# Kernel optimization log

Measured on AMD Instinct MI355X. Metric: run time of the kernel, lower is better.

## Reference

```python
import jax, jax.numpy as jnp
import numpy as np

L = 2048  # sequence length
V = 2048  # num_tokens == channel width (one-hot embedding)
B = 4     # batch


def _pos_bias(v_table):
    # pos[i,j] = max(i-j, 0); embed via [L,1] table -> [L,L]
    i = jnp.arange(L)
    pos = jnp.maximum(i[:, None] - i[None, :], 0)
    return v_table[pos, 0]


def setup_inputs() -> dict:
    key = jax.random.key(0)
    ks = jax.random.split(key, 11)
    idx = jax.random.randint(ks[0], (B, L), 0, V)
    lin = lambda k, std: (jax.random.normal(k, (V, V), dtype=jnp.float32) * std)
    return {
        "idx": idx,
        # layer_zero: all std=1 (explicit re-init in torch code)
        "Wq0": lin(ks[1], 1.0), "Wk0": lin(ks[2], 1.0), "Wv0": lin(ks[3], 1.0),
        # layer_one: Wk std=1 (re-init), Wv std=0.02 (default init); Wq is zero-fn
        "Wk1": lin(ks[4], 1.0), "Wv1": lin(ks[5], 0.02),
        # layer_two: Wq,Wv std=1 (re-init), Wk std=0.02 (default)
        "Wq2": lin(ks[6], 1.0), "Wk2": lin(ks[7], 0.02), "Wv2": lin(ks[8], 1.0),
        # relative-position embedding tables [L,1], std=0.02
        "v0": jax.random.normal(ks[9], (L, 1), dtype=jnp.float32) * 0.02,
        "v1": jax.random.normal(ks[10], (L, 1), dtype=jnp.float32) * 0.02,
    }


def reference(idx, Wq0, Wk0, Wv0, Wk1, Wv1, Wq2, Wk2, Wv2, v0, v1):
    e = jax.nn.one_hot(idx, V, dtype=jnp.float32)            # [B,L,V]
    tril = jnp.tril(jnp.ones((L, L), dtype=bool))
    p0 = _pos_bias(v0)                                       # [L,L]
    p1 = _pos_bias(v1)

    # layer_zero(e, e): scores = Q@K^T + sum_e(K)[:,None]*pos, tril, @V (no softmax)
    K0 = e @ Wk0.T
    Q0 = e @ Wq0.T
    V0 = e @ Wv0.T
    s0 = jnp.einsum('bqv,bkv->bqk', Q0, K0) + K0.sum(-1)[:, :, None] * p0[None]
    l0 = jnp.where(tril, s0, 0.0) @ V0                       # [B,L,V]

    # layer_one(l0, e): Wq is zero-fn -> only the pos-bias term survives
    K1 = e @ Wk1.T
    V1 = l0 @ Wv1.T
    s1 = K1.sum(-1)[:, :, None] * p1[None]
    l1 = jnp.where(tril, s1, 0.0) @ V1

    # layer_two(e, l1): v is zero-fn -> no pos bias
    K2 = l1 @ Wk2.T
    Q2 = e @ Wq2.T
    V2 = e @ Wv2.T
    s2 = jnp.einsum('bqv,bkv->bqk', Q2, K2)
    logits = jnp.where(tril, s2, 0.0) @ V2                   # [B,L,V]
    return logits
```

## Files before the change

kernel.cpp:

```cpp
#include <hip/hip_runtime.h>

typedef float f32x4 __attribute__((ext_vector_type(4)));
typedef short s16x8 __attribute__((ext_vector_type(8)));

constexpr int L = 2048;
constexpr int V = 2048;
constexpr int NB = 4;
constexpr size_t VV  = (size_t)V * V;
constexpr size_t BLV = (size_t)NB * L * V;
constexpr size_t LV  = (size_t)L * V;

__device__ __forceinline__ unsigned short f2bf(float f) {
    unsigned u = __float_as_uint(f);
    u = (u + 0x7FFFu + ((u >> 16) & 1u)) >> 16;
    return (unsigned short)u;
}
__device__ __forceinline__ float bf2f(unsigned short s) {
    return __uint_as_float(((unsigned)s) << 16);
}

__device__ __forceinline__ void gload16(const unsigned short* g, unsigned short* l) {
    auto gp = (const __attribute__((address_space(1))) unsigned int*)g;
    auto lp = (__attribute__((address_space(3))) unsigned int*)l;
    __builtin_amdgcn_global_load_lds(gp, lp, 16, 0, 0);
}


__device__ __forceinline__ void stage2(const unsigned short* A, const unsigned short* B,
                                       int m0, int n0, int k0, unsigned short* buf,
                                       int wave, int lane) {
    int rl = lane >> 2, csl = lane & 3;
    #pragma unroll
    for (int h = 0; h < 2; ++h) {
        int rr = wave * 32 + h * 16;
        int row = rr + rl;
        int ch = csl ^ ((row >> 1) & 3);
        size_t ga = (size_t)row * 2048 + k0 + ch * 8;
        gload16(A + (size_t)m0 * 2048 + ga, buf + rr * 32);
        gload16(B + (size_t)n0 * 2048 + ga, buf + 8192 + rr * 32);
    }
}

__device__ __forceinline__ s16x8 frag(const unsigned short* arr, int row, int kc) {
    int cs = kc ^ ((row >> 1) & 3);
    return *(const s16x8*)&arr[row * 32 + cs * 8];
}

__device__ __forceinline__ void kloop(const unsigned short* Ab, const unsigned short* Bb,
                                      int m0, int n0, int NKB, unsigned short* lds,
                                      int wave, int lane, int wr, int wc,
                                      f32x4 (&acc)[8][4]) {
    const int r15 = lane & 15, kc = lane >> 4;

    stage2(Ab, Bb, m0, n0, 0,  lds,         wave, lane);
    stage2(Ab, Bb, m0, n0, 32, lds + 16384, wave, lane);
    stage2(Ab, Bb, m0, n0, 64, lds + 32768, wave, lane);
    asm volatile("s_waitcnt vmcnt(8)" ::: "memory");
    __builtin_amdgcn_sched_barrier(0);
    __builtin_amdgcn_s_barrier();
    __builtin_amdgcn_sched_barrier(0);

    for (int t = 0; t < NKB; ++t) {
        const unsigned short* cur = lds + (t & 3) * 16384;
        unsigned short* nxt = lds + ((t + 3) & 3) * 16384;
        const int rem = NKB - 1 - t;

        s16x8 bfr[4], afr[4];
        #pragma unroll
        for (int nf = 0; nf < 4; ++nf)
            bfr[nf] = frag(cur + 8192, wc * 64 + nf * 16 + r15, kc);
        #pragma unroll
        for (int mf = 0; mf < 4; ++mf)
            afr[mf] = frag(cur, wr * 128 + mf * 16 + r15, kc);
        if (rem >= 3)
            stage2(Ab, Bb, m0, n0, (t + 3) * 32, nxt, wave, lane);
        __builtin_amdgcn_sched_barrier(0);
        __builtin_amdgcn_s_barrier();
        __builtin_amdgcn_sched_barrier(0);
        __builtin_amdgcn_s_setprio(1);
        #pragma unroll
        for (int mf = 0; mf < 4; ++mf)
            #pragma unroll
            for (int nf = 0; nf < 4; ++nf)
                acc[mf][nf] = __builtin_amdgcn_mfma_f32_16x16x32_bf16(afr[mf], bfr[nf], acc[mf][nf], 0, 0, 0);
        __builtin_amdgcn_s_setprio(0);
        __builtin_amdgcn_sched_barrier(0);
        __builtin_amdgcn_s_barrier();
        __builtin_amdgcn_sched_barrier(0);

        s16x8 afr2[4];
        #pragma unroll
        for (int mf = 0; mf < 4; ++mf)
            afr2[mf] = frag(cur, wr * 128 + (mf + 4) * 16 + r15, kc);
        __builtin_amdgcn_sched_barrier(0);
        __builtin_amdgcn_s_barrier();
        __builtin_amdgcn_sched_barrier(0);
        __builtin_amdgcn_s_setprio(1);
        #pragma unroll
        for (int mf = 0; mf < 4; ++mf)
            #pragma unroll
            for (int nf = 0; nf < 4; ++nf)
                acc[mf + 4][nf] = __builtin_amdgcn_mfma_f32_16x16x32_bf16(afr2[mf], bfr[nf], acc[mf + 4][nf], 0, 0, 0);
        __builtin_amdgcn_s_setprio(0);
        __builtin_amdgcn_sched_barrier(0);
        if (rem >= 3)      { asm volatile("s_waitcnt vmcnt(8)" ::: "memory"); }
        else if (rem == 2) { asm volatile("s_waitcnt vmcnt(4)" ::: "memory"); }
        else if (rem == 1) { asm volatile("s_waitcnt vmcnt(0)" ::: "memory"); }
        __builtin_amdgcn_s_barrier();
        __builtin_amdgcn_sched_barrier(0);
    }
}

template<int OUTM, bool TOEP>
__global__ __launch_bounds__(512, 2) void gemm_big(
    const unsigned short* __restrict__ A, size_t sA,
    const unsigned short* __restrict__ B, size_t sB,
    float* __restrict__ outF, unsigned short* __restrict__ outH, size_t sO,
    const int* __restrict__ idxp, const float* __restrict__ ks)
{
    __shared__ __align__(16) unsigned short lds[4 * 16384];

    const int tid  = threadIdx.x;
    const int lane = tid & 63, wave = tid >> 6;
    const int wr = wave >> 2, wc = wave & 3;
    const int bz = blockIdx.z;
    int bx = blockIdx.x, by = blockIdx.y;
    if constexpr (TOEP) { int tswap = bx; bx = by; by = tswap; }
    const int m0 = by * 256, n0 = bx * 256;
    const int r15 = lane & 15, kc = lane >> 4;

    const unsigned short* Ab = A + (size_t)bz * sA;
    const unsigned short* Bb = B + (size_t)bz * sB;
    const int NKB = TOEP ? 8 * (bx + 1) : 64;

    f32x4 acc[8][4];
    const f32x4 zf = {0.f, 0.f, 0.f, 0.f};
    #pragma unroll
    for (int i = 0; i < 8; ++i)
        #pragma unroll
        for (int j = 0; j < 4; ++j) acc[i][j] = zf;

    kloop(Ab, Bb, m0, n0, NKB, lds, wave, lane, wr, wc, acc);

    float csc[4];
    if constexpr (TOEP) {
        #pragma unroll
        for (int nf = 0; nf < 4; ++nf) {
            int gcol = n0 + wc * 64 + nf * 16 + r15;
            csc[nf] = ks[idxp[bz * L + gcol]];
        }
    }
    #pragma unroll
    for (int mf = 0; mf < 8; ++mf) {
        #pragma unroll
        for (int r = 0; r < 4; ++r) {
            int grow = m0 + wr * 128 + mf * 16 + kc * 4 + r;
            #pragma unroll
            for (int nf = 0; nf < 4; ++nf) {
                float v = acc[mf][nf][r];
                if constexpr (TOEP) v *= csc[nf];
                int gcol = n0 + wc * 64 + nf * 16 + r15;
                size_t o = (size_t)bz * sO + (size_t)grow * 2048 + gcol;
                if constexpr (OUTM == 0) outF[o] = v;
                else                     outH[o] = f2bf(v);
            }
        }
    }
}

struct PDesc { const unsigned short* A; const unsigned short* B; float* oF; unsigned short* oH; };

__global__ __launch_bounds__(512, 2) void gemm_pre_big(PDesc d0, PDesc d1, PDesc d2) {
    PDesc d = (blockIdx.z == 0) ? d0 : (blockIdx.z == 1) ? d1 : d2;
    __shared__ __align__(16) unsigned short lds[4 * 16384];

    const int tid  = threadIdx.x;
    const int lane = tid & 63, wave = tid >> 6;
    const int wr = wave >> 2, wc = wave & 3;
    const int m0 = blockIdx.y * 256, n0 = blockIdx.x * 256;
    const int r15 = lane & 15, kc = lane >> 4;

    f32x4 acc[8][4];
    const f32x4 zf = {0.f, 0.f, 0.f, 0.f};
    #pragma unroll
    for (int i = 0; i < 8; ++i)
        #pragma unroll
        for (int j = 0; j < 4; ++j) acc[i][j] = zf;

    kloop(d.A, d.B, m0, n0, 64, lds, wave, lane, wr, wc, acc);

    const bool isF = (d.oF != nullptr);
    #pragma unroll
    for (int mf = 0; mf < 8; ++mf) {
        #pragma unroll
        for (int r = 0; r < 4; ++r) {
            int grow = m0 + wr * 128 + mf * 16 + kc * 4 + r;
            #pragma unroll
            for (int nf = 0; nf < 4; ++nf) {
                float v = acc[mf][nf][r];
                int gcol = n0 + wc * 64 + nf * 16 + r15;
                size_t o = (size_t)grow * 2048 + gcol;
                if (isF) d.oF[o] = v;
                else     d.oH[o] = f2bf(v);
            }
        }
    }
}

__global__ __launch_bounds__(512, 2) void gemm_preK(const unsigned short* __restrict__ A,
                                                    const unsigned short* __restrict__ B,
                                                    float* __restrict__ outP) {
    __shared__ __align__(16) unsigned short lds[4 * 16384];

    const int tid  = threadIdx.x;
    const int lane = tid & 63, wave = tid >> 6;
    const int wr = wave >> 2, wc = wave & 3;
    const int m0 = blockIdx.y * 256, n0 = blockIdx.x * 256;
    const int r15 = lane & 15, kc = lane >> 4;
    const int z = blockIdx.z;

    const unsigned short* Ab = A + z * 512;
    const unsigned short* Bb = B + z * 512;
    float* outF = outP + (size_t)z * VV;

    f32x4 acc[8][4];
    const f32x4 zf = {0.f, 0.f, 0.f, 0.f};
    #pragma unroll
    for (int i = 0; i < 8; ++i)
        #pragma unroll
        for (int j = 0; j < 4; ++j) acc[i][j] = zf;

    kloop(Ab, Bb, m0, n0, 16, lds, wave, lane, wr, wc, acc);

    #pragma unroll
    for (int mf = 0; mf < 8; ++mf) {
        #pragma unroll
        for (int r = 0; r < 4; ++r) {
            int grow = m0 + wr * 128 + mf * 16 + kc * 4 + r;
            #pragma unroll
            for (int nf = 0; nf < 4; ++nf) {
                int gcol = n0 + wc * 64 + nf * 16 + r15;
                outF[(size_t)grow * 2048 + gcol] = acc[mf][nf][r];
            }
        }
    }
}

__global__ __launch_bounds__(256) void reduce4_cast(const float* __restrict__ P,
                                                    unsigned short* __restrict__ H) {
    int i = blockIdx.x * 256 + threadIdx.x;
    const float4* p0 = (const float4*)P;
    const float4* p1 = (const float4*)(P + VV);
    const float4* p2 = (const float4*)(P + 2 * VV);
    const float4* p3 = (const float4*)(P + 3 * VV);
    float4 a = p0[i], b = p1[i], c = p2[i], d = p3[i];
    ushort4 h;
    h.x = f2bf(a.x + b.x + c.x + d.x);
    h.y = f2bf(a.y + b.y + c.y + d.y);
    h.z = f2bf(a.z + b.z + c.z + d.z);
    h.w = f2bf(a.w + b.w + c.w + d.w);
    ((ushort4*)H)[i] = h;
}


__global__ __launch_bounds__(256) void colsum_atomic(const float* __restrict__ W,
                                                     float* __restrict__ out) {
    int r0 = blockIdx.x * 8;
    int c = threadIdx.x;
    float s[8];
    #pragma unroll
    for (int i = 0; i < 8; ++i) s[i] = 0.f;
    for (int r = 0; r < 8; ++r) {
        const float* row = W + (size_t)(r0 + r) * V;
        #pragma unroll
        for (int i = 0; i < 8; ++i) s[i] += row[c + i * 256];
    }
    #pragma unroll
    for (int i = 0; i < 8; ++i) atomicAdd(&out[c + i * 256], s[i]);
}

__global__ void init_kernel(float* __restrict__ ks0, float* __restrict__ ks1) {
    int i = blockIdx.x * 256 + threadIdx.x;
    if (i < 2048) { ks0[i] = 0.f; ks1[i] = 0.f; }
}

__global__ __launch_bounds__(256) void tb_fill(const float* __restrict__ v1,
                                               unsigned short* __restrict__ TBh) {
    int n = blockIdx.x;
    int c0 = threadIdx.x * 8;
    s16x8 hv;
    #pragma unroll
    for (int i = 0; i < 8; ++i) {
        int k = c0 + i;
        float f = (k <= n) ? v1[n - k] : 0.f;
        hv[i] = (short)f2bf(f);
    }
    *(s16x8*)&TBh[(size_t)n * 2048 + c0] = hv;
}

struct TDesc { const float* A; unsigned short* Th; };

__global__ void transpose_cast_multi(TDesc d0, TDesc d1, TDesc d2, TDesc d3, TDesc d4) {
    TDesc d;
    switch (blockIdx.z) {
        case 0: d = d0; break;
        case 1: d = d1; break;
        case 2: d = d2; break;
        case 3: d = d3; break;
        default: d = d4; break;
    }
    __shared__ float tile[32][33];
    int x = blockIdx.x * 32 + threadIdx.x;
    int y0 = blockIdx.y * 32;
    for (int r = threadIdx.y; r < 32; r += 8)
        tile[r][threadIdx.x] = d.A[(size_t)(y0 + r) * V + x];
    __syncthreads();
    int xo = blockIdx.y * 32 + threadIdx.x;
    int yo0 = blockIdx.x * 32;
    for (int r = threadIdx.y; r < 32; r += 8)
        d.Th[(size_t)(yo0 + r) * V + xo] = f2bf(tile[threadIdx.x][r]);
}

__global__ __launch_bounds__(256) void cast_kernel(const float* __restrict__ A,
                                                   unsigned short* __restrict__ H,
                                                   int n4) {
    int i = blockIdx.x * 256 + threadIdx.x;
    if (i >= n4) return;
    float4 f = ((const float4*)A)[i];
    ushort4 h;
    h.x = f2bf(f.x); h.y = f2bf(f.y); h.z = f2bf(f.z); h.w = f2bf(f.w);
    ((ushort4*)H)[i] = h;
}


__global__ __launch_bounds__(256) void scatterA_kernel(const int* __restrict__ idx,
                                                       const float* __restrict__ G0,
                                                       const float* __restrict__ ks0,
                                                       const float* __restrict__ v0,
                                                       unsigned short* __restrict__ Th) {
    __shared__ float buck[4 * 2048];
    int tid = threadIdx.x;
    const float4 z4 = make_float4(0.f, 0.f, 0.f, 0.f);
    #pragma unroll
    for (int i = 0; i < 8; ++i) ((float4*)buck)[tid + i * 256] = z4;
    __syncthreads();

    int b = blockIdx.y, q0 = blockIdx.x * 4;
    int qr = tid >> 6, lane = tid & 63;
    int q = q0 + qr;
    const int* idxb = idx + b * L;
    int iq = idxb[q];
    float kq = ks0[iq];
    const float* Grow = G0 + (size_t)iq * V;
    float* brow = buck + qr * 2048;

    int k = lane;
    for (; k + 192 <= q; k += 256) {
        int i0 = idxb[k], i1 = idxb[k + 64], i2 = idxb[k + 128], i3 = idxb[k + 192];
        float g0 = Grow[i0], g1 = Grow[i1], g2 = Grow[i2], g3 = Grow[i3];
        float w0 = v0[q - k], w1 = v0[q - k - 64], w2 = v0[q - k - 128], w3 = v0[q - k - 192];
        atomicAdd(&brow[i0], g0 + kq * w0);
        atomicAdd(&brow[i1], g1 + kq * w1);
        atomicAdd(&brow[i2], g2 + kq * w2);
        atomicAdd(&brow[i3], g3 + kq * w3);
    }
    for (; k <= q; k += 64) {
        int ik = idxb[k];
        atomicAdd(&brow[ik], Grow[ik] + kq * v0[q - k]);
    }
    __syncthreads();
    size_t base = ((size_t)b * L + q0) * V;
    #pragma unroll
    for (int it = 0; it < 4; ++it) {
        int i = tid + it * 256;
        s16x8 hv;
        #pragma unroll
        for (int j = 0; j < 8; ++j) hv[j] = (short)f2bf(buck[i * 8 + j]);
        *(s16x8*)&Th[base + (size_t)i * 8] = hv;
    }
}

__global__ __launch_bounds__(256) void scatterC_kernel(const int* __restrict__ idx,
                                                       const unsigned short* __restrict__ T2h,
                                                       unsigned short* __restrict__ Th) {
    __shared__ float buck[4 * 2048];
    int tid = threadIdx.x;
    const float4 z4 = make_float4(0.f, 0.f, 0.f, 0.f);
    #pragma unroll
    for (int i = 0; i < 8; ++i) ((float4*)buck)[tid + i * 256] = z4;
    __syncthreads();

    int b = blockIdx.y, q0 = blockIdx.x * 4;
    int qr = tid >> 6, lane = tid & 63;
    int q = q0 + qr;
    const int* idxb = idx + b * L;
    int iq = idxb[q];
    const unsigned short* Trow = T2h + ((size_t)b * V + iq) * L;
    float* brow = buck + qr * 2048;

    int k = lane;
    for (; k + 192 <= q; k += 256) {
        int i0 = idxb[k], i1 = idxb[k + 64], i2 = idxb[k + 128], i3 = idxb[k + 192];
        float t0 = bf2f(Trow[k]), t1 = bf2f(Trow[k + 64]);
        float t2 = bf2f(Trow[k + 128]), t3 = bf2f(Trow[k + 192]);
        atomicAdd(&brow[i0], t0);
        atomicAdd(&brow[i1], t1);
        atomicAdd(&brow[i2], t2);
        atomicAdd(&brow[i3], t3);
    }
    for (; k <= q; k += 64)
        atomicAdd(&brow[idxb[k]], bf2f(Trow[k]));
    __syncthreads();
    size_t base = ((size_t)b * L + q0) * V;
    #pragma unroll
    for (int it = 0; it < 4; ++it) {
        int i = tid + it * 256;
        s16x8 hv;
        #pragma unroll
        for (int j = 0; j < 8; ++j) hv[j] = (short)f2bf(buck[i * 8 + j]);
        *(s16x8*)&Th[base + (size_t)i * 8] = hv;
    }
}


extern "C" void kernel_launch(void* const* d_in, const int* in_sizes, int n_in,
                              void* d_out, int out_size, void* d_ws, size_t ws_size,
                              hipStream_t stream) {
    (void)in_sizes; (void)n_in; (void)out_size; (void)ws_size;
    const int*   idx = (const int*)d_in[0];
    const float* Wq0 = (const float*)d_in[1];
    const float* Wk0 = (const float*)d_in[2];
    const float* Wv0 = (const float*)d_in[3];
    const float* Wk1 = (const float*)d_in[4];
    const float* Wv1 = (const float*)d_in[5];
    const float* Wq2 = (const float*)d_in[6];
    const float* Wk2 = (const float*)d_in[7];
    const float* Wv2 = (const float*)d_in[8];
    const float* v0  = (const float*)d_in[9];
    const float* v1  = (const float*)d_in[10];
    float* out = (float*)d_out;

    char* W = (char*)d_ws;
    const size_t MiB = 1024 * 1024;

    unsigned short* PPT = (unsigned short*)W;
    unsigned short* TAh = (unsigned short*)W;
    unsigned short* T2h = (unsigned short*)W;
    float* Rp = (float*)(W + 8 * MiB);
    unsigned short* Y1 = (unsigned short*)(W + 64 * MiB);
    unsigned short* Y2 = (unsigned short*)(W + 72 * MiB);
    unsigned short* Uh  = (unsigned short*)(W + 64 * MiB);
    unsigned short* TCh = Uh;
    float* Gf = (float*)(W + 96 * MiB);
    unsigned short* Y4 = (unsigned short*)(W + 112 * MiB);
    unsigned short* X1 = (unsigned short*)(W + 128 * MiB);
    unsigned short* X2 = (unsigned short*)(W + 136 * MiB);
    unsigned short* X3 = (unsigned short*)(W + 144 * MiB);
    unsigned short* X4 = (unsigned short*)(W + 152 * MiB);
    unsigned short* TBh = X3;
    float* ks0 = (float*)(W + 192 * MiB);
    float* ks1 = (float*)(W + 192 * MiB + 16 * 1024);

    dim3 blk(256);

    {
        TDesc t0{Wq0, X1}, t1{Wk0, X2}, t2{Wq2, X3}, t3{Wk2, X4}, t4{Wv0, Y1};
        transpose_cast_multi<<<dim3(64, 64, 5), dim3(32, 8), 0, stream>>>(t0, t1, t2, t3, t4);
    }
    cast_kernel<<<dim3((int)(VV / 4 / 256)), blk, 0, stream>>>(Wv1, Y2, (int)(VV / 4));
    init_kernel<<<dim3(8), blk, 0, stream>>>(ks0, ks1);
    colsum_atomic<<<dim3(256), blk, 0, stream>>>(Wk0, ks0);
    colsum_atomic<<<dim3(256), blk, 0, stream>>>(Wk1, ks1);

    {
        PDesc dG{X1, X2, Gf, nullptr};
        PDesc dM{X3, X4, nullptr, Y4};
        PDesc dP{Y1, Y2, nullptr, PPT};
        gemm_pre_big<<<dim3(8, 8, 3), dim3(512), 0, stream>>>(dG, dM, dP);
    }
    tb_fill<<<dim3(2048), blk, 0, stream>>>(v1, TBh);
    gemm_preK<<<dim3(8, 8, 4), dim3(512), 0, stream>>>(Y4, PPT, Rp);
    reduce4_cast<<<dim3((int)(VV / 4 / 256)), blk, 0, stream>>>(Rp, X1);

    scatterA_kernel<<<dim3(L / 4, NB), blk, 0, stream>>>(idx, Gf, ks0, v0, TAh);

    gemm_big<1, false><<<dim3(8, 8, NB), dim3(512), 0, stream>>>(
        X1, 0, TAh, LV, nullptr, Uh, LV, nullptr, nullptr);

    gemm_big<1, true><<<dim3(8, 8, NB), dim3(512), 0, stream>>>(
        Uh, LV, TBh, 0, nullptr, T2h, LV, idx, ks1);

    scatterC_kernel<<<dim3(L / 4, NB), blk, 0, stream>>>(idx, T2h, TCh);

    cast_kernel<<<dim3((int)(VV / 4 / 256)), blk, 0, stream>>>(Wv2, X2, (int)(VV / 4));

    gemm_big<0, false><<<dim3(8, 32, 1), dim3(512), 0, stream>>>(
        TCh, 0, X2, 0, out, nullptr, 0, nullptr, nullptr);
}
```

Measured before the change: 491.0 us.

## Restructure GEMM main loop to double-buffered K=64 tiles with staggered staging

Replaces the 4-stage K=32 LDS ring with a 2-stage buffer of K=64 tiles, each split into two 32-wide slices. Global-to-LDS loads for the next tile are spread across the four MFMA phases of the current tile, and the swizzle is changed to row&3. The goal is fewer loop iterations and barriers per unit of K and better overlap of loads with MFMA work. The trade-off is shallower prefetch depth, since only one tile is in flight ahead, so memory latency may be less well hidden.

```diff
diff --git a/kernel.cpp b/kernel.cpp
--- a/kernel.cpp
+++ b/kernel.cpp
@@ -25,89 +25,112 @@
     __builtin_amdgcn_global_load_lds(gp, lp, 16, 0, 0);
 }
 
-
-__device__ __forceinline__ void stage2(const unsigned short* A, const unsigned short* B,
-                                       int m0, int n0, int k0, unsigned short* buf,
-                                       int wave, int lane) {
-    int rl = lane >> 2, csl = lane & 3;
-    #pragma unroll
-    for (int h = 0; h < 2; ++h) {
-        int rr = wave * 32 + h * 16;
-        int row = rr + rl;
-        int ch = csl ^ ((row >> 1) & 3);
-        size_t ga = (size_t)row * 2048 + k0 + ch * 8;
-        gload16(A + (size_t)m0 * 2048 + ga, buf + rr * 32);
-        gload16(B + (size_t)n0 * 2048 + ga, buf + 8192 + rr * 32);
-    }
-}
-
-__device__ __forceinline__ s16x8 frag(const unsigned short* arr, int row, int kc) {
-    int cs = kc ^ ((row >> 1) & 3);
-    return *(const s16x8*)&arr[row * 32 + cs * 8];
-}
-
-__device__ __forceinline__ void kloop(const unsigned short* Ab, const unsigned short* Bb,
-                                      int m0, int n0, int NKB, unsigned short* lds,
-                                      int wave, int lane, int wr, int wc,
-                                      f32x4 (&acc)[8][4]) {
+#define SBAR __builtin_amdgcn_sched_barrier(0)
+
+
+__device__ __forceinline__ void stage_half(const unsigned short* G, int r0, int k0, int s,
+                                           unsigned short* slice, int wave, int lane) {
+    int rl = lane >> 2, slot = lane & 3;
+    #pragma unroll
+    for (int r = 0; r < 2; ++r) {
+        int rowl = r * 128 + wave * 16 + rl;
+        int colg = k0 + s * 32 + ((slot ^ (rowl & 3)) * 8);
+        gload16(G + (size_t)(r0 + rowl) * 2048 + colg,
+                slice + (size_t)(r * 128 + wave * 16) * 32);
+    }
+}
+
+__device__ __forceinline__ s16x8 frag64(const unsigned short* slice, int row, int kc) {
+    return *(const s16x8*)&slice[row * 32 + ((kc ^ (row & 3)) * 8)];
+}
+
+__device__ __forceinline__ void kloop64(const unsigned short* Ab, const unsigned short* Bb,
+                                        int m0, int n0, int NT, unsigned short* lds,
+                                        int wave, int lane, int wr, int wc,
+                                        f32x4 (&acc)[8][4]) {
     const int r15 = lane & 15, kc = lane >> 4;
 
-    stage2(Ab, Bb, m0, n0, 0,  lds,         wave, lane);
-    stage2(Ab, Bb, m0, n0, 32, lds + 16384, wave, lane);
-    stage2(Ab, Bb, m0, n0, 64, lds + 32768, wave, lane);
-    asm volatile("s_waitcnt vmcnt(8)" ::: "memory");
-    __builtin_amdgcn_sched_barrier(0);
-    __builtin_amdgcn_s_barrier();
-    __builtin_amdgcn_sched_barrier(0);
-
-    for (int t = 0; t < NKB; ++t) {
-        const unsigned short* cur = lds + (t & 3) * 16384;
-        unsigned short* nxt = lds + ((t + 3) & 3) * 16384;
-        const int rem = NKB - 1 - t;
-
-        s16x8 bfr[4], afr[4];
+    stage_half(Ab, m0, 0, 0, lds + 0,     wave, lane);
+    stage_half(Bb, n0, 0, 0, lds + 16384, wave, lane);
+    stage_half(Ab, m0, 0, 1, lds + 8192,  wave, lane);
+    stage_half(Bb, n0, 0, 1, lds + 24576, wave, lane);
+    asm volatile("s_waitcnt vmcnt(4)" ::: "memory");
+    SBAR; __builtin_amdgcn_s_barrier(); SBAR;
+
+    for (int t = 0; t < NT; ++t) {
+        unsigned short* cur = lds + (t & 1) * 32768;
+        unsigned short* nxt = lds + ((t + 1) & 1) * 32768;
+        const bool pre = (t + 1 < NT);
+        const int k1 = (t + 1) * 64;
+
+        s16x8 b0[4], b1[4], a[4];
+
         #pragma unroll
         for (int nf = 0; nf < 4; ++nf)
-            bfr[nf] = frag(cur + 8192, wc * 64 + nf * 16 + r15, kc);
-        #pragma unroll
-        for (int mf = 0; mf < 4; ++mf)
-            afr[mf] = frag(cur, wr * 128 + mf * 16 + r15, kc);
-        if (rem >= 3)
-            stage2(Ab, Bb, m0, n0, (t + 3) * 32, nxt, wave, lane);
-        __builtin_amdgcn_sched_barrier(0);
-        __builtin_amdgcn_s_barrier();
-        __builtin_amdgcn_sched_barrier(0);
+            b0[nf] = frag64(cur + 16384, wc * 64 + nf * 16 + r15, kc);
+        #pragma unroll
+        for (int mf = 0; mf < 4; ++mf)
+            a[mf] = frag64(cur, wr * 128 + mf * 16 + r15, kc);
+        if (pre) stage_half(Ab, m0, k1, 0, nxt, wave, lane);
+        SBAR; __builtin_amdgcn_s_barrier(); SBAR;
         __builtin_amdgcn_s_setprio(1);
         #pragma unroll
         for (int mf = 0; mf < 4; ++mf)
             #pragma unroll
             for (int nf = 0; nf < 4; ++nf)
-                acc[mf][nf] = __builtin_amdgcn_mfma_f32_16x16x32_bf16(afr[mf], bfr[nf], acc[mf][nf], 0, 0, 0);
+                acc[mf][nf] = __builtin_amdgcn_mfma_f32_16x16x32_bf16(a[mf], b0[nf], acc[mf][nf], 0, 0, 0);
         __builtin_amdgcn_s_setprio(0);
-        __builtin_amdgcn_sched_barrier(0);
-        __builtin_amdgcn_s_barrier();
-        __builtin_amdgcn_sched_barrier(0);
-
-        s16x8 afr2[4];
-        #pragma unroll
-        for (int mf = 0; mf < 4; ++mf)
-            afr2[mf] = frag(cur, wr * 128 + (mf + 4) * 16 + r15, kc);
-        __builtin_amdgcn_sched_barrier(0);
-        __builtin_amdgcn_s_barrier();
-        __builtin_amdgcn_sched_barrier(0);
+        SBAR; __builtin_amdgcn_s_barrier(); SBAR;
+
+        #pragma unroll
+        for (int mf = 0; mf < 4; ++mf)
+            a[mf] = frag64(cur, wr * 128 + (mf + 4) * 16 + r15, kc);
+        if (pre) stage_half(Bb, n0, k1, 0, nxt + 16384, wave, lane);
+        SBAR; __builtin_amdgcn_s_barrier(); SBAR;
         __builtin_amdgcn_s_setprio(1);
         #pragma unroll
         for (int mf = 0; mf < 4; ++mf)
             #pragma unroll
             for (int nf = 0; nf < 4; ++nf)
-                acc[mf + 4][nf] = __builtin_amdgcn_mfma_f32_16x16x32_bf16(afr2[mf], bfr[nf], acc[mf + 4][nf], 0, 0, 0);
+                acc[mf + 4][nf] = __builtin_amdgcn_mfma_f32_16x16x32_bf16(a[mf], b0[nf], acc[mf + 4][nf], 0, 0, 0);
         __builtin_amdgcn_s_setprio(0);
-        __builtin_amdgcn_sched_barrier(0);
-        if (rem >= 3)      { asm volatile("s_waitcnt vmcnt(8)" ::: "memory"); }
-        else if (rem == 2) { asm volatile("s_waitcnt vmcnt(4)" ::: "memory"); }
-        else if (rem == 1) { asm volatile("s_waitcnt vmcnt(0)" ::: "memory"); }
-        __builtin_amdgcn_s_barrier();
-        __builtin_amdgcn_sched_barrier(0);
+        SBAR;
+        if (pre) { asm volatile("s_waitcnt vmcnt(4)" ::: "memory"); }
+        else     { asm volatile("s_waitcnt vmcnt(0)" ::: "memory"); }
+        SBAR; __builtin_amdgcn_s_barrier(); SBAR;
+
+        #pragma unroll
+        for (int nf = 0; nf < 4; ++nf)
+            b1[nf] = frag64(cur + 24576, wc * 64 + nf * 16 + r15, kc);
+        #pragma unroll
+        for (int mf = 0; mf < 4; ++mf)
+            a[mf] = frag64(cur + 8192, wr * 128 + mf * 16 + r15, kc);
+        if (pre) stage_half(Ab, m0, k1, 1, nxt + 8192, wave, lane);
+        SBAR; __builtin_amdgcn_s_barrier(); SBAR;
+        __builtin_amdgcn_s_setprio(1);
+        #pragma unroll
+        for (int mf = 0; mf < 4; ++mf)
+            #pragma unroll
+            for (int nf = 0; nf < 4; ++nf)
+                acc[mf][nf] = __builtin_amdgcn_mfma_f32_16x16x32_bf16(a[mf], b1[nf], acc[mf][nf], 0, 0, 0);
+        __builtin_amdgcn_s_setprio(0);
+        SBAR; __builtin_amdgcn_s_barrier(); SBAR;
+
+        #pragma unroll
+        for (int mf = 0; mf < 4; ++mf)
+            a[mf] = frag64(cur + 8192, wr * 128 + (mf + 4) * 16 + r15, kc);
+        if (pre) stage_half(Bb, n0, k1, 1, nxt + 24576, wave, lane);
+        SBAR; __builtin_amdgcn_s_barrier(); SBAR;
+        __builtin_amdgcn_s_setprio(1);
+        #pragma unroll
+        for (int mf = 0; mf < 4; ++mf)
+            #pragma unroll
+            for (int nf = 0; nf < 4; ++nf)
+                acc[mf + 4][nf] = __builtin_amdgcn_mfma_f32_16x16x32_bf16(a[mf], b1[nf], acc[mf + 4][nf], 0, 0, 0);
+        __builtin_amdgcn_s_setprio(0);
+        SBAR;
+        if (pre) { asm volatile("s_waitcnt vmcnt(4)" ::: "memory"); }
+        SBAR; __builtin_amdgcn_s_barrier(); SBAR;
     }
 }
 
@@ -118,7 +141,7 @@
     float* __restrict__ outF, unsigned short* __restrict__ outH, size_t sO,
     const int* __restrict__ idxp, const float* __restrict__ ks)
 {
-    __shared__ __align__(16) unsigned short lds[4 * 16384];
+    __shared__ __align__(16) unsigned short lds[2 * 32768];
 
     const int tid  = threadIdx.x;
     const int lane = tid & 63, wave = tid >> 6;
@@ -131,7 +154,7 @@
 
     const unsigned short* Ab = A + (size_t)bz * sA;
     const unsigned short* Bb = B + (size_t)bz * sB;
-    const int NKB = TOEP ? 8 * (bx + 1) : 64;
+    const int NT = TOEP ? 4 * (bx + 1) : 32;
 
     f32x4 acc[8][4];
     const f32x4 zf = {0.f, 0.f, 0.f, 0.f};
@@ -140,7 +163,7 @@
         #pragma unroll
         for (int j = 0; j < 4; ++j) acc[i][j] = zf;
 
-    kloop(Ab, Bb, m0, n0, NKB, lds, wave, lane, wr, wc, acc);
+    kloop64(Ab, Bb, m0, n0, NT, lds, wave, lane, wr, wc, acc);
 
     float csc[4];
     if constexpr (TOEP) {
@@ -172,7 +195,7 @@
 
 __global__ __launch_bounds__(512, 2) void gemm_pre_big(PDesc d0, PDesc d1, PDesc d2) {
     PDesc d = (blockIdx.z == 0) ? d0 : (blockIdx.z == 1) ? d1 : d2;
-    __shared__ __align__(16) unsigned short lds[4 * 16384];
+    __shared__ __align__(16) unsigned short lds[2 * 32768];
 
     const int tid  = threadIdx.x;
     const int lane = tid & 63, wave = tid >> 6;
@@ -187,7 +210,7 @@
         #pragma unroll
         for (int j = 0; j < 4; ++j) acc[i][j] = zf;
 
-    kloop(d.A, d.B, m0, n0, 64, lds, wave, lane, wr, wc, acc);
+    kloop64(d.A, d.B, m0, n0, 32, lds, wave, lane, wr, wc, acc);
 
     const bool isF = (d.oF != nullptr);
     #pragma unroll
@@ -210,7 +233,7 @@
 __global__ __launch_bounds__(512, 2) void gemm_preK(const unsigned short* __restrict__ A,
                                                     const unsigned short* __restrict__ B,
                                                     float* __restrict__ outP) {
-    __shared__ __align__(16) unsigned short lds[4 * 16384];
+    __shared__ __align__(16) unsigned short lds[2 * 32768];
 
     const int tid  = threadIdx.x;
     const int lane = tid & 63, wave = tid >> 6;
@@ -230,7 +253,7 @@
         #pragma unroll
         for (int j = 0; j < 4; ++j) acc[i][j] = zf;
 
-    kloop(Ab, Bb, m0, n0, 16, lds, wave, lane, wr, wc, acc);
+    kloop64(Ab, Bb, m0, n0, 8, lds, wave, lane, wr, wc, acc);
 
     #pragma unroll
     for (int mf = 0; mf < 8; ++mf) {
```

Result: no change. 497.9 us (+1.4%).
